# Kernel optimization log

Hardware: AMD Instinct MI355X
Metric: run time of the kernel (lower is better)

## Reference

```python
import jax, jax.numpy as jnp
import numpy as np

N = 50000      # nodes
E = 800000     # edges (avg degree 16)
G = 128        # g_dim (input feature dim)
H1 = 128       # h1_dim (RGCN output dim)
H2 = 32        # h2_dim (per-head channels)
HEADS = 4
R = 6          # num_relations
OUT = H2 * HEADS  # 128, BatchNorm width
BN_EPS = 1e-5


def setup_inputs() -> dict:
    key = jax.random.key(0)
    k = jax.random.split(key, 16)
    s = 0.05
    return {
        "node_features": jax.random.normal(k[0], (N, G), jnp.float32),
        "node_type": jax.random.randint(k[1], (N,), 0, 3),
        "edge_index": jax.random.randint(k[2], (2, E), 0, N),
        "edge_type": jax.random.randint(k[3], (E,), 0, R),
        # RGCNConv params (root_weight=True, bias=True, aggr='mean')
        "W_rel": jax.random.normal(k[4], (R, G, H1), jnp.float32) * s,
        "W_root": jax.random.normal(k[5], (G, H1), jnp.float32) * s,
        "b_rgcn": jnp.zeros((H1,), jnp.float32),
        # TransformerConv params (concat=True, root_weight=True via lin_skip)
        "Wq": jax.random.normal(k[6], (H1, OUT), jnp.float32) * s,
        "bq": jnp.zeros((OUT,), jnp.float32),
        "Wk": jax.random.normal(k[7], (H1, OUT), jnp.float32) * s,
        "bk": jnp.zeros((OUT,), jnp.float32),
        "Wv": jax.random.normal(k[8], (H1, OUT), jnp.float32) * s,
        "bv": jnp.zeros((OUT,), jnp.float32),
        "Wskip": jax.random.normal(k[9], (H1, OUT), jnp.float32) * s,
        "bskip": jnp.zeros((OUT,), jnp.float32),
        # BatchNorm1d affine params
        "bn_gamma": jnp.ones((OUT,), jnp.float32),
        "bn_beta": jnp.zeros((OUT,), jnp.float32),
    }


def _gnn_forward(node_features, edge_index, edge_type,
                 W_rel, W_root, b_rgcn,
                 Wq, bq, Wk, bk, Wv, bv, Wskip, bskip,
                 bn_gamma, bn_beta):
    src, dst = edge_index[0], edge_index[1]  # message flows src (j) -> dst (i)

    # ---- RGCNConv with mean aggregation per relation ----
    # Transform all nodes under every relation: [R, N, H1]
    xt = jnp.einsum('nd,rdo->rno', node_features, W_rel)
    msg = xt[edge_type, src]                          # [E, H1]
    seg = edge_type * N + dst                         # composite (relation, dst) segment id
    agg = jax.ops.segment_sum(msg, seg, num_segments=R * N).reshape(R, N, H1)
    cnt = jax.ops.segment_sum(jnp.ones((E,), msg.dtype), seg,
                              num_segments=R * N).reshape(R, N)
    x = node_features @ W_root + b_rgcn + (agg / jnp.maximum(cnt, 1.0)[:, :, None]).sum(0)

    # ---- TransformerConv (heads=HEADS, concat=True) ----
    q = (x @ Wq + bq).reshape(N, HEADS, H2)
    kk = (x @ Wk + bk).reshape(N, HEADS, H2)
    v = (x @ Wv + bv).reshape(N, HEADS, H2)

    score = (q[dst] * kk[src]).sum(-1) / np.sqrt(H2)  # [E, HEADS]
    m = jax.ops.segment_max(score, dst, num_segments=N)   # -inf for isolated nodes
    m = jnp.where(jnp.isfinite(m), m, 0.0)
    ex = jnp.exp(score - m[dst])
    den = jax.ops.segment_sum(ex, dst, num_segments=N)
    alpha = ex / (den[dst] + 1e-16)                   # [E, HEADS]

    out = jax.ops.segment_sum(alpha[:, :, None] * v[src], dst,
                              num_segments=N).reshape(N, OUT)
    out = out + x @ Wskip + bskip                     # skip / root connection

    # ---- BatchNorm1d (training-mode batch stats) + LeakyReLU(0.01) ----
    mu = out.mean(0)
    var = out.var(0)  # biased, as torch uses for normalization
    y = (out - mu) * jax.lax.rsqrt(var + BN_EPS) * bn_gamma + bn_beta
    return jax.nn.leaky_relu(y, negative_slope=0.01)


def reference(node_features, node_type, edge_index, edge_type,
              W_rel, W_root, b_rgcn,
              Wq, bq, Wk, bk, Wv, bv, Wskip, bskip,
              bn_gamma, bn_beta):
    # node_type is accepted but unused, matching the original forward.
    return _gnn_forward(node_features, edge_index, edge_type,
                        W_rel, W_root, b_rgcn,
                        Wq, bq, Wk, bk, Wv, bv, Wskip, bskip,
                        bn_gamma, bn_beta)
```

## Files before the change

### kernel.cpp

```cpp
#include <hip/hip_runtime.h>
#include <hip/hip_fp16.h>
#include <stdint.h>

#define G      128
#define OUTW   128
#define RNUM   6

typedef unsigned short us;
typedef _Float16 f16x8 __attribute__((ext_vector_type(8)));
typedef float    f32x4 __attribute__((ext_vector_type(4)));

__device__ inline float h2f(us u) { __half h; *(us*)&h = u; return __half2float(h); }
__device__ inline us f2h(float f) { __half h = __float2half(f); return *(us*)&h; }
__device__ inline float2 h22(int u) { return __half22float2(*(__half2*)&u); }

union FragU { f16x8 v; ushort4 u[2]; };

__global__ void count_kernel(const int* __restrict__ ei, const int* __restrict__ et,
                             int* __restrict__ segcnt, int N, int E) {
    int e = blockIdx.x * blockDim.x + threadIdx.x;
    if (e >= E) return;
    int dst = ei[E + e];
    int r   = et[e];
    atomicAdd(&segcnt[dst * RNUM + r], 1);
}

__global__ __launch_bounds__(256)
void scan_part(const int* __restrict__ cnt, int* __restrict__ bsum, int n) {
    __shared__ int s[256];
    int base = blockIdx.x * 1024, t = threadIdx.x;
    int v = 0;
    for (int j = 0; j < 4; ++j) { int idx = base + j * 256 + t; if (idx < n) v += cnt[idx]; }
    s[t] = v; __syncthreads();
    for (int off = 128; off; off >>= 1) { if (t < off) s[t] += s[t + off]; __syncthreads(); }
    if (!t) bsum[blockIdx.x] = s[0];
}

__global__ __launch_bounds__(512)
void scan_top(const int* __restrict__ bsum, int* __restrict__ boff,
              int* __restrict__ segptr, int nb, int n) {
    __shared__ int s[512];
    int t = threadIdx.x;
    int v = (t < nb) ? bsum[t] : 0;
    s[t] = v;
    __syncthreads();
    for (int off = 1; off < 512; off <<= 1) {
        int y = (t >= off) ? s[t - off] : 0;
        __syncthreads();
        s[t] += y;
        __syncthreads();
    }
    if (t < nb) boff[t + 1] = s[t];
    if (!t) boff[0] = 0;
    if (t == nb - 1) segptr[n] = s[t];
}

__global__ __launch_bounds__(256)
void scan_apply(const int* __restrict__ cnt, const int* __restrict__ boff,
                int* __restrict__ segptr, int* __restrict__ cursor, int n) {
    __shared__ int L[1024];
    __shared__ int SS[256];
    int base = blockIdx.x * 1024, t = threadIdx.x;
    for (int j = 0; j < 4; ++j) { int idx = base + j * 256 + t; L[j * 256 + t] = (idx < n) ? cnt[idx] : 0; }
    __syncthreads();
    int s0 = L[t*4] + L[t*4+1] + L[t*4+2] + L[t*4+3];
    SS[t] = s0; __syncthreads();
    for (int off = 1; off < 256; off <<= 1) {
        int y = (t >= off) ? SS[t - off] : 0;
        __syncthreads();
        SS[t] += y;
        __syncthreads();
    }
    int e0 = (t ? SS[t - 1] : 0) + boff[blockIdx.x];
    int4 ov;
    int a;
    a = L[t*4+0]; ov.x = e0; e0 += a;
    a = L[t*4+1]; ov.y = e0; e0 += a;
    a = L[t*4+2]; ov.z = e0; e0 += a;
    a = L[t*4+3]; ov.w = e0; e0 += a;
    int idx0 = base + t * 4;
    if (idx0 + 3 < n) {
        *(int4*)(segptr + idx0) = ov;
        *(int4*)(cursor + idx0) = ov;
    } else {
        int vals[4] = {ov.x, ov.y, ov.z, ov.w};
        for (int k = 0; k < 4; ++k)
            if (idx0 + k < n) { segptr[idx0 + k] = vals[k]; cursor[idx0 + k] = vals[k]; }
    }
}

__global__ void scatter_kernel(const int* __restrict__ ei, const int* __restrict__ et,
                               int* __restrict__ cursor, unsigned* __restrict__ esrc,
                               int N, int E) {
    int e = blockIdx.x * blockDim.x + threadIdx.x;
    if (e >= E) return;
    int src = ei[e];
    int dst = ei[E + e];
    int r   = et[e];
    int pos = atomicAdd(&cursor[dst * RNUM + r], 1);
    esrc[pos] = (unsigned)src;
}

__global__ __launch_bounds__(256)
void prep_kernel(const float* __restrict__ x, us* __restrict__ xh,
                 const float* __restrict__ Wrel, const float* __restrict__ Wroot,
                 ushort4* __restrict__ Btr,
                 const float* __restrict__ Wq, const float* __restrict__ Wk,
                 const float* __restrict__ Wv, const float* __restrict__ Ws,
                 ushort4* __restrict__ Btq, int xblocks) {
    int b = blockIdx.x;
    if (b < xblocks) {
        int i = b * 256 + threadIdx.x;
        float4 a = ((const float4*)x)[2*i];
        float4 c = ((const float4*)x)[2*i+1];
        ushort4 u0 = { f2h(a.x), f2h(a.y), f2h(a.z), f2h(a.w) };
        ushort4 u1 = { f2h(c.x), f2h(c.y), f2h(c.z), f2h(c.w) };
        ((ushort4*)xh)[2*i]   = u0;
        ((ushort4*)xh)[2*i+1] = u1;
    } else if (b < xblocks + 112) {
        int idx = (b - xblocks) * 256 + threadIdx.x;
        int kq = idx >> 7, n = idx & 127;
        ushort4 o;
        us* op = (us*)&o;
#pragma unroll
        for (int i = 0; i < 4; ++i) {
            int k = 4 * kq + i;
            float v = (k < 768) ? Wrel[(size_t)k * 128 + n] : Wroot[(size_t)(k - 768) * 128 + n];
            op[i] = f2h(v);
        }
        Btr[idx] = o;
    } else {
        int idx = (b - xblocks - 112) * 256 + threadIdx.x;
        int kq = idx >> 9, n = idx & 511;
        int quad = n >> 7, nl = n & 127;
        const float* W = (quad == 0) ? Wq : (quad == 1) ? Wk : (quad == 2) ? Wv : Ws;
        ushort4 o;
        us* op = (us*)&o;
#pragma unroll
        for (int i = 0; i < 4; ++i) {
            int k = 4 * kq + i;
            op[i] = f2h(W[(size_t)k * 128 + nl]);
        }
        Btq[idx] = o;
    }
}

__global__ __launch_bounds__(256)
void agg_kernel(const us* __restrict__ xh, const int* __restrict__ segptr,
                const unsigned* __restrict__ esrc, us* __restrict__ meanF, int N) {
    const int wv = threadIdx.x >> 6, l = threadIdx.x & 63;
    const int i = blockIdx.x * 4 + wv;
    if (i >= N) return;
    const int t = i >> 4, row = i & 15;
    const int e0 = __builtin_amdgcn_readfirstlane(segptr[i * RNUM]);
    const int e1 = __builtin_amdgcn_readfirstlane(segptr[i * RNUM + RNUM]);

    int rcur = 0;
    int sstart = e0;
    int bnext = __builtin_amdgcn_readfirstlane(segptr[i * RNUM + 1]);
    float2 a = {0.f, 0.f};
    us* wbase = meanF + (size_t)t * 12288 + row * 4 + (l & 1) * 2;
    const int kqo = (l >> 1) * 64;

#define FLUSH() { \
    float sc_ = 1.f / fmaxf((float)(bnext - sstart), 1.f); \
    ushort2 t2_ = { f2h(a.x * sc_), f2h(a.y * sc_) }; \
    *(ushort2*)(wbase + rcur * 2048 + kqo) = t2_; \
    a.x = 0.f; a.y = 0.f; \
    sstart = bnext; ++rcur; \
    if (rcur < RNUM) bnext = __builtin_amdgcn_readfirstlane(segptr[i * RNUM + rcur + 1]); }

#define GET(J) ((unsigned)__shfl((int)pv, (J)))
#define LX(Q)  (*(const ushort2*)(xh + (size_t)(Q) * G + 2 * l))
#define STEP(U) { while (p >= bnext && rcur < RNUM - 1) FLUSH(); \
                  a.x += h2f((U).x); a.y += h2f((U).y); ++p; }

    int p = e0;
    for (int wb = e0; wb < e1; wb += 64) {
        const int nc = min(64, e1 - wb);
        unsigned pv = (wb + l < e1) ? esrc[wb + l] : 0u;
        int j = 0;
        while (j + 8 <= nc) {
            unsigned q0 = GET(j+0), q1 = GET(j+1), q2 = GET(j+2), q3 = GET(j+3);
            unsigned q4 = GET(j+4), q5 = GET(j+5), q6 = GET(j+6), q7 = GET(j+7);
            ushort2 u0 = LX(q0), u1 = LX(q1), u2 = LX(q2), u3 = LX(q3);
            ushort2 u4 = LX(q4), u5 = LX(q5), u6 = LX(q6), u7 = LX(q7);
            STEP(u0); STEP(u1); STEP(u2); STEP(u3);
            STEP(u4); STEP(u5); STEP(u6); STEP(u7);
            j += 8;
        }
        while (j + 2 <= nc) {
            unsigned q0 = GET(j), q1 = GET(j+1);
            ushort2 u0 = LX(q0), u1 = LX(q1);
            STEP(u0); STEP(u1);
            j += 2;
        }
        if (j < nc) {
            unsigned q0 = GET(j);
            ushort2 u0 = LX(q0);
            STEP(u0);
            ++j;
        }
    }
    while (rcur < RNUM) FLUSH();
#undef STEP
#undef LX
#undef GET
#undef FLUSH
}

__global__ __launch_bounds__(256)
void rgcn_mfma3(const us* __restrict__ xh, const us* __restrict__ meanF,
                const ushort4* __restrict__ Btr, const float* __restrict__ brg,
                us* __restrict__ xrh, int N) {
    const int tid = threadIdx.x;
    const int w = tid >> 6, l = tid & 63;
    const int lh = l >> 4, lm = l & 15;
    const int rowbase = blockIdx.x * 128 + w * 32;
    const int ntile = N >> 4;

    const us* amean[2];
    const us* aroot[2];
#pragma unroll
    for (int tt = 0; tt < 2; ++tt) {
        int t  = min((rowbase >> 4) + tt, ntile - 1);
        int gr = min(rowbase + tt * 16 + lm, N - 1);
        amean[tt] = meanF + (size_t)t * 12288 + lm * 4;
        aroot[tt] = xh + (size_t)gr * 128;
    }

    f32x4 acc[2][8];
#pragma unroll
    for (int tt = 0; tt < 2; ++tt)
#pragma unroll
        for (int ct = 0; ct < 8; ++ct) {
            float b = brg[ct * 16 + lm];
            acc[tt][ct] = (f32x4){b, b, b, b};
        }

    for (int s = 0; s < 24; ++s) {
        const int kqg = s * 8 + lh;
        const ushort4* B0 = Btr + (size_t)kqg * 128 + lm;
        const ushort4* B1 = B0 + 4 * 128;
        FragU bf[8];
#pragma unroll
        for (int ct = 0; ct < 8; ++ct) { bf[ct].u[0] = B0[ct * 16]; bf[ct].u[1] = B1[ct * 16]; }
#pragma unroll
        for (int tt = 0; tt < 2; ++tt) {
            FragU af;
            af.u[0] = *(const ushort4*)(amean[tt] + kqg * 64);
            af.u[1] = *(const ushort4*)(amean[tt] + (kqg + 4) * 64);
#pragma unroll
            for (int ct = 0; ct < 8; ++ct)
                acc[tt][ct] = __builtin_amdgcn_mfma_f32_16x16x32_f16(af.v, bf[ct].v, acc[tt][ct], 0, 0, 0);
        }
    }
#pragma unroll
    for (int s = 0; s < 4; ++s) {
        const int kql = s * 8 + lh;
        const int kqg = 192 + kql;
        const ushort4* B0 = Btr + (size_t)kqg * 128 + lm;
        const ushort4* B1 = B0 + 4 * 128;
        FragU bf[8];
#pragma unroll
        for (int ct = 0; ct < 8; ++ct) { bf[ct].u[0] = B0[ct * 16]; bf[ct].u[1] = B1[ct * 16]; }
#pragma unroll
        for (int tt = 0; tt < 2; ++tt) {
            FragU af;
            af.u[0] = *(const ushort4*)(aroot[tt] + kql * 4);
            af.u[1] = *(const ushort4*)(aroot[tt] + kql * 4 + 16);
#pragma unroll
            for (int ct = 0; ct < 8; ++ct)
                acc[tt][ct] = __builtin_amdgcn_mfma_f32_16x16x32_f16(af.v, bf[ct].v, acc[tt][ct], 0, 0, 0);
        }
    }

#pragma unroll
    for (int tt = 0; tt < 2; ++tt)
#pragma unroll
        for (int ct = 0; ct < 8; ++ct)
#pragma unroll
            for (int i = 0; i < 4; ++i) {
                int r = rowbase + tt * 16 + 4 * lh + i;
                if (r < N) xrh[(size_t)r * 128 + ct * 16 + lm] = f2h(acc[tt][ct][i]);
            }
}

__global__ __launch_bounds__(256)
void qkvs_mfma3(const us* __restrict__ xrh, const ushort4* __restrict__ Btq,
                const float* __restrict__ bq, const float* __restrict__ bk,
                const float* __restrict__ bv, const float* __restrict__ bs,
                us* __restrict__ qsh, us* __restrict__ kvh, int N) {
    const int tid = threadIdx.x;
    const int quad = tid >> 6, l = tid & 63;
    const int lh = l >> 4, lm = l & 15;
    const int base = blockIdx.x * 32;
    const float* bias = (quad == 0) ? bq : (quad == 1) ? bk : (quad == 2) ? bv : bs;

    const us* ap[2];
#pragma unroll
    for (int tt = 0; tt < 2; ++tt) {
        int ar = min(base + tt * 16 + lm, N - 1);
        ap[tt] = xrh + (size_t)ar * 128;
    }

    f32x4 acc[2][8];
#pragma unroll
    for (int tt = 0; tt < 2; ++tt)
#pragma unroll
        for (int ct = 0; ct < 8; ++ct) {
            float b = bias[ct * 16 + lm];
            acc[tt][ct] = (f32x4){b, b, b, b};
        }

#pragma unroll
    for (int s = 0; s < 4; ++s) {
        const int kq = s * 8 + lh;
        const ushort4* B0 = Btq + (size_t)kq * 512 + quad * 128 + lm;
        const ushort4* B1 = B0 + 4 * 512;
        FragU bf[8];
#pragma unroll
        for (int ct = 0; ct < 8; ++ct) { bf[ct].u[0] = B0[ct * 16]; bf[ct].u[1] = B1[ct * 16]; }
#pragma unroll
        for (int tt = 0; tt < 2; ++tt) {
            FragU af;
            af.u[0] = *(const ushort4*)(ap[tt] + kq * 4);
            af.u[1] = *(const ushort4*)(ap[tt] + kq * 4 + 16);
#pragma unroll
            for (int ct = 0; ct < 8; ++ct)
                acc[tt][ct] = __builtin_amdgcn_mfma_f32_16x16x32_f16(af.v, bf[ct].v, acc[tt][ct], 0, 0, 0);
        }
    }

    if (quad == 0 || quad == 3) {
        const int off = (quad == 0) ? 0 : 128;
#pragma unroll
        for (int tt = 0; tt < 2; ++tt)
#pragma unroll
            for (int ct = 0; ct < 8; ++ct)
#pragma unroll
                for (int i = 0; i < 4; ++i) {
                    int r = base + tt * 16 + 4 * lh + i;
                    if (r < N) qsh[(size_t)r * 256 + off + ct * 16 + lm] = f2h(acc[tt][ct][i]);
                }
    } else {
        const int off = (quad == 1) ? 0 : 2;
#pragma unroll
        for (int tt = 0; tt < 2; ++tt)
#pragma unroll
            for (int ct = 0; ct < 8; ++ct)
#pragma unroll
                for (int i = 0; i < 4; ++i) {
                    int r = base + tt * 16 + 4 * lh + i;
                    int col = ct * 16 + lm;
                    if (r < N) kvh[(size_t)r * 256 + (col >> 1) * 4 + (col & 1) + off] = f2h(acc[tt][ct][i]);
                }
    }
}

__global__ __launch_bounds__(256)
void attn_kernel(const us* __restrict__ qsh, const us* __restrict__ kvh,
                 const int* __restrict__ segptr, const unsigned* __restrict__ esrc,
                 float* __restrict__ out, float* __restrict__ bnS,
                 float* __restrict__ bnQ, int N) {
    __shared__ float sS[128], sQ[128];
    const int tid = threadIdx.x;
    if (tid < 128) { sS[tid] = 0.f; sQ[tid] = 0.f; }
    __syncthreads();

    const int wv = tid >> 6, l = tid & 63;
    const int hh = l >> 5, ll = l & 31;
    const int stride = gridDim.x * 8;
    const float QS = 0.17677669529663687f;
    float4 bsum = {0,0,0,0}, bsq = {0,0,0,0};

#define SCORE(D, S) { \
    float2 ka_ = h22((D).x), kb_ = h22((D).z); \
    float t_ = q4.x*ka_.x + q4.y*ka_.y + q4.z*kb_.x + q4.w*kb_.y; \
    t_ += __shfl_xor(t_, 1, 8); t_ += __shfl_xor(t_, 2, 8); t_ += __shfl_xor(t_, 4, 8); \
    S = t_; }

    for (int ibase = blockIdx.x * 8 + wv * 2; ibase < N; ibase += stride) {
        const bool act = (ibase + hh) < N;
        const int i = min(ibase + hh, N - 1);

        int2 qu = *(const int2*)(qsh + (size_t)i * 256 + 4 * ll);
        float2 qa = h22(qu.x), qb = h22(qu.y);
        float4 q4 = { qa.x * QS, qa.y * QS, qb.x * QS, qb.y * QS };

        float m = -INFINITY, den = 0.f;
        float4 acc = {0,0,0,0};
        const int e0 = segptr[(size_t)i * RNUM], e1 = segptr[(size_t)i * RNUM + RNUM];

        for (int wb = e0; wb < e1; wb += 32) {
            const int nc = min(32, e1 - wb);
            unsigned pv = (wb + ll < e1) ? esrc[wb + ll] : 0u;
            int j = 0;
            for (; j + 4 <= nc; j += 4) {
                unsigned p0 = (unsigned)__shfl((int)pv, j+0, 32);
                unsigned p1 = (unsigned)__shfl((int)pv, j+1, 32);
                unsigned p2 = (unsigned)__shfl((int)pv, j+2, 32);
                unsigned p3 = (unsigned)__shfl((int)pv, j+3, 32);
                int4 d0 = *(const int4*)(kvh + (size_t)p0 * 256 + 8 * ll);
                int4 d1 = *(const int4*)(kvh + (size_t)p1 * 256 + 8 * ll);
                int4 d2 = *(const int4*)(kvh + (size_t)p2 * 256 + 8 * ll);
                int4 d3 = *(const int4*)(kvh + (size_t)p3 * 256 + 8 * ll);
                float s0, s1, s2, s3;
                SCORE(d0, s0); SCORE(d1, s1); SCORE(d2, s2); SCORE(d3, s3);
                float mx = fmaxf(m, fmaxf(fmaxf(s0, s1), fmaxf(s2, s3)));
                float rs = __expf(m - mx);
                float w0 = __expf(s0 - mx), w1 = __expf(s1 - mx);
                float w2 = __expf(s2 - mx), w3 = __expf(s3 - mx);
                den = den * rs + ((w0 + w1) + (w2 + w3));
                float2 va0 = h22(d0.y), vb0 = h22(d0.w);
                float2 va1 = h22(d1.y), vb1 = h22(d1.w);
                float2 va2 = h22(d2.y), vb2 = h22(d2.w);
                float2 va3 = h22(d3.y), vb3 = h22(d3.w);
                acc.x = acc.x * rs + w0*va0.x + w1*va1.x + w2*va2.x + w3*va3.x;
                acc.y = acc.y * rs + w0*va0.y + w1*va1.y + w2*va2.y + w3*va3.y;
                acc.z = acc.z * rs + w0*vb0.x + w1*vb1.x + w2*vb2.x + w3*vb3.x;
                acc.w = acc.w * rs + w0*vb0.y + w1*vb1.y + w2*vb2.y + w3*vb3.y;
                m = mx;
            }
            for (; j < nc; ++j) {
                unsigned p0 = (unsigned)__shfl((int)pv, j, 32);
                int4 d0 = *(const int4*)(kvh + (size_t)p0 * 256 + 8 * ll);
                float s0; SCORE(d0, s0);
                float mx = fmaxf(m, s0);
                float rs = __expf(m - mx);
                float w0 = __expf(s0 - mx);
                den = den * rs + w0;
                float2 va0 = h22(d0.y), vb0 = h22(d0.w);
                acc.x = acc.x * rs + w0 * va0.x;
                acc.y = acc.y * rs + w0 * va0.y;
                acc.z = acc.z * rs + w0 * vb0.x;
                acc.w = acc.w * rs + w0 * vb0.y;
                m = mx;
            }
        }

        float inv = 1.f / (den + 1e-16f);
        int2 su = *(const int2*)(qsh + (size_t)i * 256 + 128 + 4 * ll);
        float2 sa = h22(su.x), sb = h22(su.y);
        float4 o = { acc.x * inv + sa.x, acc.y * inv + sa.y,
                     acc.z * inv + sb.x, acc.w * inv + sb.y };
        if (act) {
            *(float4*)(out + (size_t)i * OUTW + 4 * ll) = o;
            bsum.x += o.x; bsum.y += o.y; bsum.z += o.z; bsum.w += o.w;
            bsq.x += o.x*o.x; bsq.y += o.y*o.y; bsq.z += o.z*o.z; bsq.w += o.w*o.w;
        }
    }
#undef SCORE

    atomicAdd(&sS[4*ll + 0], bsum.x);
    atomicAdd(&sS[4*ll + 1], bsum.y);
    atomicAdd(&sS[4*ll + 2], bsum.z);
    atomicAdd(&sS[4*ll + 3], bsum.w);
    atomicAdd(&sQ[4*ll + 0], bsq.x);
    atomicAdd(&sQ[4*ll + 1], bsq.y);
    atomicAdd(&sQ[4*ll + 2], bsq.z);
    atomicAdd(&sQ[4*ll + 3], bsq.w);
    __syncthreads();
    if (tid < 128) {
        atomicAdd(&bnS[tid], sS[tid]);
        atomicAdd(&bnQ[tid], sQ[tid]);
    }
}

__global__ __launch_bounds__(256)
void apply_kernel(float* __restrict__ out, const float* __restrict__ bnS,
                  const float* __restrict__ bnQ, const float* __restrict__ gamma,
                  const float* __restrict__ beta, int N, int total4) {
    __shared__ float A_s[128], B_s[128];
    const int tid = threadIdx.x;
    if (tid < 128) {
        float fN  = (float)N;
        float mu  = bnS[tid] / fN;
        float var = bnQ[tid] / fN - mu * mu;
        float rv  = rsqrtf(var + 1e-5f);
        float A   = rv * gamma[tid];
        A_s[tid] = A;
        B_s[tid] = beta[tid] - mu * A;
    }
    __syncthreads();
    for (int idx4 = blockIdx.x * 256 + tid; idx4 < total4; idx4 += gridDim.x * 256) {
        float4 v = ((const float4*)out)[idx4];
        int c0 = (idx4 * 4) & 127;
        float y;
        y = A_s[c0    ] * v.x + B_s[c0    ]; v.x = (y > 0.f) ? y : 0.01f * y;
        y = A_s[c0 + 1] * v.y + B_s[c0 + 1]; v.y = (y > 0.f) ? y : 0.01f * y;
        y = A_s[c0 + 2] * v.z + B_s[c0 + 2]; v.z = (y > 0.f) ? y : 0.01f * y;
        y = A_s[c0 + 3] * v.w + B_s[c0 + 3]; v.w = (y > 0.f) ? y : 0.01f * y;
        ((float4*)out)[idx4] = v;
    }
}

static inline char* alignp(char* p) {
    return (char*)(((uintptr_t)p + 255) & ~(uintptr_t)255);
}

extern "C" void kernel_launch(void* const* d_in, const int* in_sizes, int n_in,
                              void* d_out, int out_size, void* d_ws, size_t ws_size,
                              hipStream_t stream) {
    const float* x     = (const float*)d_in[0];
    const int*   ei    = (const int*)  d_in[2];
    const int*   et    = (const int*)  d_in[3];
    const float* Wrel  = (const float*)d_in[4];
    const float* Wroot = (const float*)d_in[5];
    const float* brg   = (const float*)d_in[6];
    const float* Wq    = (const float*)d_in[7];
    const float* bq    = (const float*)d_in[8];
    const float* Wk    = (const float*)d_in[9];
    const float* bk    = (const float*)d_in[10];
    const float* Wv    = (const float*)d_in[11];
    const float* bv    = (const float*)d_in[12];
    const float* Wsk   = (const float*)d_in[13];
    const float* bsk   = (const float*)d_in[14];
    const float* gamma = (const float*)d_in[15];
    const float* beta  = (const float*)d_in[16];
    float* out = (float*)d_out;

    const int N = in_sizes[0] / G;
    const int E = in_sizes[3];
    const int NSEG = N * RNUM;
    const int NB_SCAN = (NSEG + 1023) / 1024;

    char* w = (char*)d_ws;
    int* segcnt = (int*)w;           w += (size_t)NSEG * 4;
    float* bnS = (float*)w;          w += 128 * 4;
    float* bnQ = (float*)w;          w += 128 * 4;
    size_t zero_bytes = (size_t)(w - (char*)d_ws);
    w = alignp(w);
    int* bsum  = (int*)w;            w += 512 * 4;
    int* boff  = (int*)w;            w += 513 * 4;
    w = alignp(w);
    int* segptr = (int*)w;           w += (size_t)(NSEG + 1) * 4;
    w = alignp(w);
    int* cursor = (int*)w;           w += (size_t)NSEG * 4;
    w = alignp(w);
    unsigned* esrc = (unsigned*)w;   w += (size_t)E * 4;
    w = alignp(w);
    us* xh     = (us*)w;             w += (size_t)N * G * 2;
    w = alignp(w);
    us* xrh    = (us*)w;             w += (size_t)N * OUTW * 2;
    w = alignp(w);
    ushort4* Btr = (ushort4*)w;      w += (size_t)224 * 128 * 8;
    w = alignp(w);
    ushort4* Btq = (ushort4*)w;      w += (size_t)32 * 512 * 8;
    w = alignp(w);
    us* meanF = (us*)w;
    us* qsh   = (us*)w;
    us* kvh   = (us*)(w + (size_t)N * 256 * 2);

    hipMemsetAsync(d_ws, 0, zero_bytes, stream);

    int eb = (E + 255) / 256;
    count_kernel<<<eb, 256, 0, stream>>>(ei, et, segcnt, N, E);

    scan_part<<<NB_SCAN, 256, 0, stream>>>(segcnt, bsum, NSEG);
    scan_top<<<1, 512, 0, stream>>>(bsum, boff, segptr, NB_SCAN, NSEG);
    scan_apply<<<NB_SCAN, 256, 0, stream>>>(segcnt, boff, segptr, cursor, NSEG);

    scatter_kernel<<<eb, 256, 0, stream>>>(ei, et, cursor, esrc, N, E);

    int xblocks = N * G / 8 / 256;
    prep_kernel<<<xblocks + 112 + 64, 256, 0, stream>>>(x, xh, Wrel, Wroot, Btr,
                                                        Wq, Wk, Wv, Wsk, Btq, xblocks);

    agg_kernel<<<(N + 3) / 4, 256, 0, stream>>>(xh, segptr, esrc, meanF, N);

    rgcn_mfma3<<<(N + 127) / 128, 256, 0, stream>>>(xh, meanF, Btr, brg, xrh, N);

    qkvs_mfma3<<<(N + 31) / 32, 256, 0, stream>>>(xrh, Btq, bq, bk, bv, bsk, qsh, kvh, N);

    attn_kernel<<<2048, 256, 0, stream>>>(qsh, kvh, segptr, esrc, out, bnS, bnQ, N);

    int total4 = N * OUTW / 4;
    apply_kernel<<<2048, 256, 0, stream>>>(out, bnS, bnQ, gamma, beta, N, total4);
}
```

Before: 453.9 us.

## Store relation means row-major and unroll attention edge loop by eight

The aggregation kernel now writes per-relation means in a plain row-major [N,768] layout instead of a tiled fragment-friendly layout, and the RGCN MFMA kernel reads A fragments directly from rows. This makes the agg writes contiguous per wave and removes the tile-clamping logic, at the cost of less contiguous fragment loads in the GEMM. Separately, the attention kernel gains an 8-edge unrolled online-softmax step ahead of the existing 4-edge loop, putting more gathers in flight at the cost of more registers.

```diff
diff --git a/kernel.cpp b/kernel.cpp
--- a/kernel.cpp
+++ b/kernel.cpp
@@ -147,11 +147,10 @@
 
 __global__ __launch_bounds__(256)
 void agg_kernel(const us* __restrict__ xh, const int* __restrict__ segptr,
-                const unsigned* __restrict__ esrc, us* __restrict__ meanF, int N) {
+                const unsigned* __restrict__ esrc, us* __restrict__ meanh, int N) {
     const int wv = threadIdx.x >> 6, l = threadIdx.x & 63;
     const int i = blockIdx.x * 4 + wv;
     if (i >= N) return;
-    const int t = i >> 4, row = i & 15;
     const int e0 = __builtin_amdgcn_readfirstlane(segptr[i * RNUM]);
     const int e1 = __builtin_amdgcn_readfirstlane(segptr[i * RNUM + RNUM]);
 
@@ -159,13 +158,12 @@
     int sstart = e0;
     int bnext = __builtin_amdgcn_readfirstlane(segptr[i * RNUM + 1]);
     float2 a = {0.f, 0.f};
-    us* wbase = meanF + (size_t)t * 12288 + row * 4 + (l & 1) * 2;
-    const int kqo = (l >> 1) * 64;
+    us* wbase = meanh + (size_t)i * 768 + 2 * l;
 
 #define FLUSH() { \
     float sc_ = 1.f / fmaxf((float)(bnext - sstart), 1.f); \
     ushort2 t2_ = { f2h(a.x * sc_), f2h(a.y * sc_) }; \
-    *(ushort2*)(wbase + rcur * 2048 + kqo) = t2_; \
+    *(ushort2*)(wbase + rcur * 128) = t2_; \
     a.x = 0.f; a.y = 0.f; \
     sstart = bnext; ++rcur; \
     if (rcur < RNUM) bnext = __builtin_amdgcn_readfirstlane(segptr[i * RNUM + rcur + 1]); }
@@ -210,23 +208,21 @@
 }
 
 __global__ __launch_bounds__(256)
-void rgcn_mfma3(const us* __restrict__ xh, const us* __restrict__ meanF,
+void rgcn_mfma4(const us* __restrict__ xh, const us* __restrict__ meanh,
                 const ushort4* __restrict__ Btr, const float* __restrict__ brg,
                 us* __restrict__ xrh, int N) {
     const int tid = threadIdx.x;
     const int w = tid >> 6, l = tid & 63;
     const int lh = l >> 4, lm = l & 15;
     const int rowbase = blockIdx.x * 128 + w * 32;
-    const int ntile = N >> 4;
-
-    const us* amean[2];
-    const us* aroot[2];
+
+    const us* am[2];
+    const us* ar[2];
 #pragma unroll
     for (int tt = 0; tt < 2; ++tt) {
-        int t  = min((rowbase >> 4) + tt, ntile - 1);
         int gr = min(rowbase + tt * 16 + lm, N - 1);
-        amean[tt] = meanF + (size_t)t * 12288 + lm * 4;
-        aroot[tt] = xh + (size_t)gr * 128;
+        am[tt] = meanh + (size_t)gr * 768;
+        ar[tt] = xh + (size_t)gr * 128;
     }
 
     f32x4 acc[2][8];
@@ -248,8 +244,8 @@
 #pragma unroll
         for (int tt = 0; tt < 2; ++tt) {
             FragU af;
-            af.u[0] = *(const ushort4*)(amean[tt] + kqg * 64);
-            af.u[1] = *(const ushort4*)(amean[tt] + (kqg + 4) * 64);
+            af.u[0] = *(const ushort4*)(am[tt] + s * 32 + 4 * lh);
+            af.u[1] = *(const ushort4*)(am[tt] + s * 32 + 4 * lh + 16);
 #pragma unroll
             for (int ct = 0; ct < 8; ++ct)
                 acc[tt][ct] = __builtin_amdgcn_mfma_f32_16x16x32_f16(af.v, bf[ct].v, acc[tt][ct], 0, 0, 0);
@@ -257,8 +253,7 @@
     }
 #pragma unroll
     for (int s = 0; s < 4; ++s) {
-        const int kql = s * 8 + lh;
-        const int kqg = 192 + kql;
+        const int kqg = 192 + s * 8 + lh;
         const ushort4* B0 = Btr + (size_t)kqg * 128 + lm;
         const ushort4* B1 = B0 + 4 * 128;
         FragU bf[8];
@@ -267,8 +262,8 @@
 #pragma unroll
         for (int tt = 0; tt < 2; ++tt) {
             FragU af;
-            af.u[0] = *(const ushort4*)(aroot[tt] + kql * 4);
-            af.u[1] = *(const ushort4*)(aroot[tt] + kql * 4 + 16);
+            af.u[0] = *(const ushort4*)(ar[tt] + s * 32 + 4 * lh);
+            af.u[1] = *(const ushort4*)(ar[tt] + s * 32 + 4 * lh + 16);
 #pragma unroll
             for (int ct = 0; ct < 8; ++ct)
                 acc[tt][ct] = __builtin_amdgcn_mfma_f32_16x16x32_f16(af.v, bf[ct].v, acc[tt][ct], 0, 0, 0);
@@ -396,6 +391,53 @@
             const int nc = min(32, e1 - wb);
             unsigned pv = (wb + ll < e1) ? esrc[wb + ll] : 0u;
             int j = 0;
+            for (; j + 8 <= nc; j += 8) {
+                unsigned p0 = (unsigned)__shfl((int)pv, j+0, 32);
+                unsigned p1 = (unsigned)__shfl((int)pv, j+1, 32);
+                unsigned p2 = (unsigned)__shfl((int)pv, j+2, 32);
+                unsigned p3 = (unsigned)__shfl((int)pv, j+3, 32);
+                unsigned p4 = (unsigned)__shfl((int)pv, j+4, 32);
+                unsigned p5 = (unsigned)__shfl((int)pv, j+5, 32);
+                unsigned p6 = (unsigned)__shfl((int)pv, j+6, 32);
+                unsigned p7 = (unsigned)__shfl((int)pv, j+7, 32);
+                int4 d0 = *(const int4*)(kvh + (size_t)p0 * 256 + 8 * ll);
+                int4 d1 = *(const int4*)(kvh + (size_t)p1 * 256 + 8 * ll);
+                int4 d2 = *(const int4*)(kvh + (size_t)p2 * 256 + 8 * ll);
+                int4 d3 = *(const int4*)(kvh + (size_t)p3 * 256 + 8 * ll);
+                int4 d4 = *(const int4*)(kvh + (size_t)p4 * 256 + 8 * ll);
+                int4 d5 = *(const int4*)(kvh + (size_t)p5 * 256 + 8 * ll);
+                int4 d6 = *(const int4*)(kvh + (size_t)p6 * 256 + 8 * ll);
+                int4 d7 = *(const int4*)(kvh + (size_t)p7 * 256 + 8 * ll);
+                float s0, s1, s2, s3, s4, s5, s6, s7;
+                SCORE(d0, s0); SCORE(d1, s1); SCORE(d2, s2); SCORE(d3, s3);
+                SCORE(d4, s4); SCORE(d5, s5); SCORE(d6, s6); SCORE(d7, s7);
+                float mx = fmaxf(m, fmaxf(
+                    fmaxf(fmaxf(s0, s1), fmaxf(s2, s3)),
+                    fmaxf(fmaxf(s4, s5), fmaxf(s6, s7))));
+                float rs = __expf(m - mx);
+                float w0 = __expf(s0 - mx), w1 = __expf(s1 - mx);
+                float w2 = __expf(s2 - mx), w3 = __expf(s3 - mx);
+                float w4 = __expf(s4 - mx), w5 = __expf(s5 - mx);
+                float w6 = __expf(s6 - mx), w7 = __expf(s7 - mx);
+                den = den * rs + (((w0 + w1) + (w2 + w3)) + ((w4 + w5) + (w6 + w7)));
+                float2 va0 = h22(d0.y), vb0 = h22(d0.w);
+                float2 va1 = h22(d1.y), vb1 = h22(d1.w);
+                float2 va2 = h22(d2.y), vb2 = h22(d2.w);
+                float2 va3 = h22(d3.y), vb3 = h22(d3.w);
+                float2 va4 = h22(d4.y), vb4 = h22(d4.w);
+                float2 va5 = h22(d5.y), vb5 = h22(d5.w);
+                float2 va6 = h22(d6.y), vb6 = h22(d6.w);
+                float2 va7 = h22(d7.y), vb7 = h22(d7.w);
+                acc.x = acc.x * rs + ((w0*va0.x + w1*va1.x) + (w2*va2.x + w3*va3.x))
+                                   + ((w4*va4.x + w5*va5.x) + (w6*va6.x + w7*va7.x));
+                acc.y = acc.y * rs + ((w0*va0.y + w1*va1.y) + (w2*va2.y + w3*va3.y))
+                                   + ((w4*va4.y + w5*va5.y) + (w6*va6.y + w7*va7.y));
+                acc.z = acc.z * rs + ((w0*vb0.x + w1*vb1.x) + (w2*vb2.x + w3*vb3.x))
+                                   + ((w4*vb4.x + w5*vb5.x) + (w6*vb6.x + w7*vb7.x));
+                acc.w = acc.w * rs + ((w0*vb0.y + w1*vb1.y) + (w2*vb2.y + w3*vb3.y))
+                                   + ((w4*vb4.y + w5*vb5.y) + (w6*vb6.y + w7*vb7.y));
+                m = mx;
+            }
             for (; j + 4 <= nc; j += 4) {
                 unsigned p0 = (unsigned)__shfl((int)pv, j+0, 32);
                 unsigned p1 = (unsigned)__shfl((int)pv, j+1, 32);
@@ -548,7 +590,7 @@
     w = alignp(w);
     ushort4* Btq = (ushort4*)w;      w += (size_t)32 * 512 * 8;
     w = alignp(w);
-    us* meanF = (us*)w;
+    us* meanh = (us*)w;
     us* qsh   = (us*)w;
     us* kvh   = (us*)(w + (size_t)N * 256 * 2);
 
@@ -567,9 +609,9 @@
     prep_kernel<<<xblocks + 112 + 64, 256, 0, stream>>>(x, xh, Wrel, Wroot, Btr,
                                                         Wq, Wk, Wv, Wsk, Btq, xblocks);
 
-    agg_kernel<<<(N + 3) / 4, 256, 0, stream>>>(xh, segptr, esrc, meanF, N);
-
-    rgcn_mfma3<<<(N + 127) / 128, 256, 0, stream>>>(xh, meanF, Btr, brg, xrh, N);
+    agg_kernel<<<(N + 3) / 4, 256, 0, stream>>>(xh, segptr, esrc, meanh, N);
+
+    rgcn_mfma4<<<(N + 127) / 128, 256, 0, stream>>>(xh, meanh, Btr, brg, xrh, N);
 
     qkvs_mfma3<<<(N + 31) / 32, 256, 0, stream>>>(xrh, Btq, bq, bk, bv, bsk, qsh, kvh, N);
 
```

New measurement: 436.9 us. 1.04x faster.
